# Performance work log

Hardware: AMD Instinct MI355X
Metric: run time of the kernel (lower is better)

## Reference

```python
import jax, jax.numpy as jnp
import numpy as np

K = 20      # kNN neighbors
H = 4       # attention heads
EPS = 1e-5  # BatchNorm eps
NEG = 0.2   # LeakyReLU negative slope


def lrelu(x):
    return jnp.where(x >= 0, x, NEG * x)


def bn(x, g, b):
    # eval-mode BatchNorm: running_mean=0, running_var=1
    return x * (g / jnp.sqrt(1.0 + EPS)) + b


def knn_idx(x):
    # x: (B, N, C) -> (B, N, K) indices of K nearest neighbors (incl. self)
    inner = -2.0 * jnp.einsum('bnc,bmc->bnm', x, x)
    xx = jnp.sum(x * x, axis=-1)
    pd = -xx[:, :, None] - inner - xx[:, None, :]  # negative squared distance
    return jax.lax.top_k(pd, K)[1]


def edge_conv(x, w, g, b):
    # EdgeConv: gather kNN features, cat(nbr-ctr, ctr), 1x1 conv, BN, LeakyReLU, max over K
    idx = knn_idx(x)                                   # (B,N,K)
    nbr = jax.vmap(lambda f, i: f[i])(x, idx)          # (B,N,K,C)
    ctr = jnp.broadcast_to(x[:, :, None, :], nbr.shape)
    e = jnp.concatenate([nbr - ctr, ctr], axis=-1)     # (B,N,K,2C)
    h = lrelu(bn(jnp.einsum('bnkc,oc->bnko', e, w), g, b))
    return jnp.max(h, axis=2)                          # (B,N,Cout)


def mha(x, w_in, b_in, w_out, b_out):
    # Faithful to source: (B,N,E) fed to nn.MultiheadAttention with batch_first=False,
    # so seq length L=B and batch=N (attention mixes across the batch axis).
    L, Nb, E = x.shape
    d = E // H
    qkv = x @ w_in.T + b_in
    q, k, v = jnp.split(qkv, 3, axis=-1)
    q = q.reshape(L, Nb, H, d) * (1.0 / np.sqrt(d))
    k = k.reshape(L, Nb, H, d)
    v = v.reshape(L, Nb, H, d)
    a = jax.nn.softmax(jnp.einsum('lnhd,mnhd->nhlm', q, k), axis=-1)
    o = jnp.einsum('nhlm,mnhd->lnhd', a, v).reshape(L, Nb, E)
    return o @ w_out.T + b_out


def setup_inputs():
    ks = iter(jax.random.split(jax.random.key(0), 64))
    def rn(shape, s=0.05):
        return jax.random.normal(next(ks), shape, jnp.float32) * s
    def gamma(c):
        return 1.0 + rn((c,), 0.1)
    B, N = 8, 1024
    inp = {'x': rn((B, N, 3), 1.0)}
    for i, (ci, co) in enumerate([(6, 64), (128, 64), (128, 128), (256, 256)], 1):
        inp[f'w{i}'] = rn((co, ci)); inp[f'g{i}'] = gamma(co); inp[f'b{i}'] = rn((co,))
    for i, e in enumerate([64, 64, 128, 256], 1):
        inp[f'a{i}_wi'] = rn((3 * e, e)); inp[f'a{i}_bi'] = rn((3 * e,))
        inp[f'a{i}_wo'] = rn((e, e));     inp[f'a{i}_bo'] = rn((e,))
    inp['w5'] = rn((1024, 512)); inp['g5'] = gamma(1024); inp['b5'] = rn((1024,))
    inp['l1w'] = rn((512, 2048)); inp['g6'] = gamma(512); inp['b6'] = rn((512,))
    inp['l2w'] = rn((256, 512)); inp['l2b'] = rn((256,))
    inp['g7'] = gamma(256); inp['b7'] = rn((256,))
    inp['l3w'] = rn((40, 256)); inp['l3b'] = rn((40,))
    return inp


def reference(x, w1, g1, b1, a1_wi, a1_bi, a1_wo, a1_bo,
              w2, g2, b2, a2_wi, a2_bi, a2_wo, a2_bo,
              w3, g3, b3, a3_wi, a3_bi, a3_wo, a3_bo,
              w4, g4, b4, a4_wi, a4_bi, a4_wo, a4_bo,
              w5, g5, b5, l1w, g6, b6, l2w, l2b, g7, b7, l3w, l3b):
    x1 = edge_conv(x, w1, g1, b1)
    x1 = mha(x1, a1_wi, a1_bi, a1_wo, a1_bo) + x1
    x2 = edge_conv(x1, w2, g2, b2)
    x2 = mha(x2, a2_wi, a2_bi, a2_wo, a2_bo) + x2
    x3 = edge_conv(x2, w3, g3, b3)
    x3 = mha(x3, a3_wi, a3_bi, a3_wo, a3_bo) + x3
    x4 = edge_conv(x3, w4, g4, b4)
    x4 = mha(x4, a4_wi, a4_bi, a4_wo, a4_bo) + x4
    h = lrelu(bn(jnp.concatenate([x1, x2, x3, x4], axis=-1) @ w5.T, g5, b5))  # (B,N,1024)
    feat = jnp.concatenate([jnp.max(h, axis=1), jnp.mean(h, axis=1)], axis=-1)  # (B,2048)
    h = lrelu(bn(feat @ l1w.T, g6, b6))
    h = lrelu(bn(h @ l2w.T + l2b, g7, b7))  # dropout is eval-mode identity
    return h @ l3w.T + l3b  # (B, 40)
```

## Files before the change

kernel.cpp:

```cpp
#include <hip/hip_runtime.h>
#include <hip/hip_bf16.h>

#define B_ 8
#define N_ 1024
#define K_ 20
#define BN_ (B_*N_)

#define BN_SCALE 0.9999950000374997f

typedef __attribute__((ext_vector_type(8))) short short8;
typedef __attribute__((ext_vector_type(4))) float f32x4;

__device__ __forceinline__ float US2F(unsigned short u) {
    union { unsigned u; float f; } c; c.u = ((unsigned)u) << 16; return c.f;
}
__device__ __forceinline__ unsigned short F2BF(float f) {
    union { float f; unsigned u; } c; c.f = f;
    unsigned r = c.u + 0x7FFF + ((c.u >> 16) & 1);
    return (unsigned short)(r >> 16);
}

__device__ __forceinline__ void ldsld16(const unsigned short* g, unsigned short* l) {
    __builtin_amdgcn_global_load_lds(
        (const __attribute__((address_space(1))) void*)g,
        (__attribute__((address_space(3))) void*)l, 16, 0, 0);
}

struct DetP { const unsigned short* g[7]; };
__device__ __forceinline__ int det_isbf(const DetP& dp) {
    int cnt = 0;
    #pragma unroll
    for (int i = 0; i < 7; i++) {
        float v = US2F(dp.g[i][0]);
        if (v > 0.5f && v < 1.5f) cnt++;
    }
    return cnt >= 4;
}

struct TPar { const void* src; void* dst; int O, I, blk0, mode; };
struct TList { TPar p[44]; };
struct TrP { const void* src; float* dst; int O, I, bx, blk0; };

__global__ __launch_bounds__(256) void k_prep(TList tl, int nent,
                                              TrP q0, TrP q1, TrP q2,
                                              int nbp, int nbtr,
                                              const void* x0, DetP dp,
                                              unsigned short* __restrict__ xa,
                                              unsigned short* __restrict__ xb,
                                              float* __restrict__ xx1) {
    __shared__ int sbf;
    if (threadIdx.x == 0) sbf = det_isbf(dp);
    __syncthreads();
    const int isbf = sbf;
    auto ld0 = [&](int idx) {
        return isbf ? US2F(((const unsigned short*)x0)[idx])
                    : ((const float*)x0)[idx];
    };
    const int bid = blockIdx.x;
    if (bid >= nbp + nbtr) {
        int blk = bid - nbp - nbtr;
        if (blk >= (BN_ * 32) / 256) {
            int i = (blk - (BN_ * 32) / 256) * 256 + threadIdx.x;
            if (i >= BN_) return;
            float s = 0.f;
            #pragma unroll
            for (int c = 0; c < 3; c++) { float v = ld0(i * 3 + c); s += v * v; }
            xx1[i] = s;
            return;
        }
        const int e = blk * 256 + threadIdx.x;
        const int i = e >> 5, p = e & 31;
        unsigned short va = 0, vb = 0;
        if (p < 9) {
            const int seg = p / 3, c = p - seg * 3;
            const float v = ld0(i * 3 + c);
            const unsigned short h = F2BF(v);
            const unsigned short l = F2BF(v - US2F(h));
            va = (seg == 1) ? l : h;
            vb = (seg < 2) ? h : l;
        }
        xa[e] = va; xb[e] = vb;
        return;
    }
    if (bid >= nbp) {
        int blk = bid - nbp;
        TrP p = q0;
        if (blk >= q2.blk0) p = q2; else if (blk >= q1.blk0) p = q1;
        blk -= p.blk0;
        const int tx = threadIdx.x & 31, ty = threadIdx.x >> 5;
        const int bi = blk % p.bx, bo = blk / p.bx;
        const int i0 = bi * 32, o0 = bo * 32;
        __shared__ float s[32][33];
        #pragma unroll
        for (int r = 0; r < 4; r++) {
            const int o = o0 + ty + r * 8, i = i0 + tx;
            if (o < p.O && i < p.I) {
                const size_t e = (size_t)o * p.I + i;
                s[ty + r * 8][tx] = isbf ? US2F(((const unsigned short*)p.src)[e])
                                         : ((const float*)p.src)[e];
            }
        }
        __syncthreads();
        #pragma unroll
        for (int r = 0; r < 4; r++) {
            const int i = i0 + ty + r * 8, o = o0 + tx;
            if (i < p.I && o < p.O) p.dst[(size_t)i * p.O + o] = s[tx][ty + r * 8];
        }
        return;
    }
    int blk = bid;
    int wi = 0;
    for (int j = nent - 1; j >= 0; j--) { if (blk >= tl.p[j].blk0) { wi = j; break; } }
    const TPar p = tl.p[wi];
    int e = (blk - p.blk0) * 256 + threadIdx.x;
    int n = p.O * p.I;
    if (e >= n) return;
    if (p.mode == 4) { ((float*)p.dst)[e] = 0.f; return; }
    int o = e / p.I, i = e - o * p.I;
    float v = isbf ? US2F(((const unsigned short*)p.src)[e])
                   : ((const float*)p.src)[e];
    if (p.mode == 0) {
        ((float*)p.dst)[(size_t)i * p.O + o] = v;
    } else if (p.mode == 2) {
        ((unsigned short*)p.dst)[e] = F2BF(v);
    } else {
        const int C = p.I >> 1;
        if (i < C) ((unsigned short*)p.dst)[(size_t)o * C + i] = F2BF(v);
        else       ((unsigned short*)p.dst)[(size_t)(p.O + o) * C + (i - C)] = F2BF(v);
    }
}

template<int KP, int TM, int TN>
__global__ __launch_bounds__(256) void k_pdm(const unsigned short* __restrict__ xa,
                                             const unsigned short* __restrict__ xb,
                                             const float* __restrict__ xx,
                                             float* __restrict__ pd) {
    const int b = blockIdx.z;
    const int rb = blockIdx.x * TM, cb = blockIdx.y * TN;
    const unsigned short* Ab = xa + (size_t)b * N_ * KP;
    const unsigned short* Bb = xb + (size_t)b * N_ * KP;
    const float* xxb = xx + (size_t)b * N_;
    const int t = threadIdx.x;
    __shared__ __align__(16) unsigned short As[2][TM * 32];
    __shared__ __align__(16) unsigned short Bs[2][TN * 32];
    const int w = t >> 6, lane = t & 63;
    constexpr int QR = TM / 2, QC = TN / 2;
    constexpr int MR = QR / 16, NR = QC / 16;
    const int wr = (w & 1) * QR, wc = (w >> 1) * QC;
    const int fr = lane & 15, q = lane >> 4;
    f32x4 acc[MR][NR] = {};

    auto STAGE = [&](int buf, int k0) {
        constexpr int AT = TM * 4;
        #pragma unroll
        for (int R = 0; R < (AT + 255) / 256; R++) {
            const int G = t + R * 256;
            if (AT >= (R + 1) * 256 || G < AT) {
                const int m = G >> 2, gs = (G & 3) ^ ((m >> 1) & 3);
                ldsld16(&Ab[(size_t)(rb + m) * KP + k0 + gs * 8], &As[buf][w * 512 + R * 2048]);
            }
        }
        constexpr int BT = TN * 4;
        #pragma unroll
        for (int R = 0; R < (BT + 255) / 256; R++) {
            const int G = t + R * 256;
            if (BT >= (R + 1) * 256 || G < BT) {
                const int n = G >> 2, gs = (G & 3) ^ ((n >> 1) & 3);
                ldsld16(&Bb[(size_t)(cb + n) * KP + k0 + gs * 8], &Bs[buf][w * 512 + R * 2048]);
            }
        }
    };

    constexpr int NT = KP / 32;
    STAGE(0, 0);
    asm volatile("s_waitcnt vmcnt(0)" ::: "memory");
    __builtin_amdgcn_s_barrier();
    int cur = 0;
    for (int ts = 0; ts < NT; ++ts) {
        if (ts + 1 < NT) STAGE(cur ^ 1, (ts + 1) * 32);
        short8 af[MR], bfr[NR];
        #pragma unroll
        for (int mi = 0; mi < MR; mi++) {
            const int r = wr + mi * 16 + fr;
            af[mi] = *reinterpret_cast<const short8*>(&As[cur][r * 32 + ((q ^ ((r >> 1) & 3)) << 3)]);
        }
        #pragma unroll
        for (int ni = 0; ni < NR; ni++) {
            const int r = wc + ni * 16 + fr;
            bfr[ni] = *reinterpret_cast<const short8*>(&Bs[cur][r * 32 + ((q ^ ((r >> 1) & 3)) << 3)]);
        }
        #pragma unroll
        for (int mi = 0; mi < MR; mi++) {
            #pragma unroll
            for (int ni = 0; ni < NR; ni++)
                acc[mi][ni] = __builtin_amdgcn_mfma_f32_16x16x32_bf16(af[mi], bfr[ni], acc[mi][ni], 0, 0, 0);
        }
        asm volatile("s_waitcnt vmcnt(0)" ::: "memory");
        __builtin_amdgcn_s_barrier();
        cur ^= 1;
    }
    float* pdb = pd + (size_t)b * N_ * N_;
    const int cr = (lane >> 4) * 4, cc = lane & 15;
    #pragma unroll
    for (int mi = 0; mi < MR; mi++) {
        #pragma unroll
        for (int ni = 0; ni < NR; ni++) {
            #pragma unroll
            for (int r = 0; r < 4; r++) {
                const int row = rb + wr + mi * 16 + cr + r;
                const int col = cb + wc + ni * 16 + cc;
                pdb[(size_t)row * N_ + col] = 2.f * acc[mi][ni][r] - xxb[col];
            }
        }
    }
}

__device__ __forceinline__ void sel_dev(const float* __restrict__ pd,
                                        int* __restrict__ idx, int blk) {
    const int w = threadIdx.x >> 6, lane = threadIdx.x & 63;
    const int i = blk * 4 + w;
    const int b = i >> 10;
    const float* row = pd + (size_t)b * N_ * N_ + (size_t)(i & 1023) * N_;
    unsigned key[16];
    #pragma unroll
    for (int q = 0; q < 16; q++) {
        const int j = q * 64 + lane;
        unsigned bits = __float_as_uint(row[j]);
        bits = (bits & 0x80000000u) ? ~bits : (bits | 0x80000000u);
        key[q] = (bits & 0xFFFFFC00u) | (unsigned)(N_ - 1 - j);
    }
    int myj = 0;
    for (int kk = 0; kk < K_; kk++) {
        unsigned m = key[0];
        #pragma unroll
        for (int u = 1; u < 16; u++) m = key[u] > m ? key[u] : m;
        #pragma unroll
        for (int s = 1; s < 64; s <<= 1) {
            unsigned o = (unsigned)__shfl_xor((int)m, s, 64);
            m = o > m ? o : m;
        }
        const int j = N_ - 1 - (int)(m & 1023u);
        if (lane == kk) myj = j;
        #pragma unroll
        for (int u = 0; u < 16; u++)
            if (key[u] == m) key[u] = 0u;
    }
    if (lane < K_) idx[(size_t)i * K_ + lane] = myj;
}

template<int KD, int NC, int TM, int TN, bool CATA, bool POOL, int SPLIT>
__device__ __forceinline__ void gemm_dev(int bx, int by,
                                         const unsigned short* __restrict__ A,
                                         const unsigned short* __restrict__ A2,
                                         const unsigned short* __restrict__ A3,
                                         const unsigned short* __restrict__ A4,
                                         const unsigned short* __restrict__ Bw,
                                         const float* __restrict__ bias,
                                         const float* __restrict__ resid,
                                         float* __restrict__ Cout,
                                         float* __restrict__ Cz, int yco,
                                         int scale_cols, float qs,
                                         const float* __restrict__ gamma,
                                         const float* __restrict__ beta,
                                         unsigned short* __restrict__ obf,
                                         unsigned* __restrict__ pmaxu,
                                         float* __restrict__ psum,
                                         unsigned short* __restrict__ sxa,
                                         unsigned short* __restrict__ sxb,
                                         float* __restrict__ xxo) {
    const int t = threadIdx.x;
    const int rb = bx * TM, cb = by * TN;
    const int w = t >> 6, lane = t & 63;
    constexpr int QR = TM / 2, QC = TN / 2;
    constexpr int MR = QR / 16, NR = QC / 16;
    const int wr = (w & 1) * QR, wc = (w >> 1) * QC;
    const int fr = lane & 15, q = lane >> 4, fq = q * 8;
    f32x4 acc[MR][NR] = {};
    if constexpr (KD % 32 == 0) {
        __shared__ __align__(16) unsigned short As[2][TM * 32];
        __shared__ __align__(16) unsigned short Bs[2][TN * 32];
        auto STAGE = [&](int buf, int k0) {
            const unsigned short* Asrc = A; int AC = KD, ac0 = k0;
            if constexpr (CATA) {
                if (k0 >= 256)      { Asrc = A4; AC = 256; ac0 = k0 - 256; }
                else if (k0 >= 128) { Asrc = A3; AC = 128; ac0 = k0 - 128; }
                else if (k0 >= 64)  { Asrc = A2; AC = 64;  ac0 = k0 - 64; }
                else                { Asrc = A;  AC = 64;  ac0 = k0; }
            }
            constexpr int AT = TM * 4;
            #pragma unroll
            for (int R = 0; R < (AT + 255) / 256; R++) {
                const int G = t + R * 256;
                if (AT >= (R + 1) * 256 || G < AT) {
                    const int m = G >> 2, gs = (G & 3) ^ ((m >> 1) & 3);
                    ldsld16(&Asrc[(size_t)(rb + m) * AC + ac0 + gs * 8], &As[buf][w * 512 + R * 2048]);
                }
            }
            constexpr int BT = TN * 4;
            #pragma unroll
            for (int R = 0; R < (BT + 255) / 256; R++) {
                const int G = t + R * 256;
                if (BT >= (R + 1) * 256 || G < BT) {
                    const int n = G >> 2, gs = (G & 3) ^ ((n >> 1) & 3);
                    ldsld16(&Bw[(size_t)(cb + n) * KD + k0 + gs * 8], &Bs[buf][w * 512 + R * 2048]);
                }
            }
        };
        constexpr int NT = KD / 32;
        STAGE(0, 0);
        asm volatile("s_waitcnt vmcnt(0)" ::: "memory");
        __builtin_amdgcn_s_barrier();
        int cur = 0;
        for (int ts = 0; ts < NT; ++ts) {
            if (ts + 1 < NT) STAGE(cur ^ 1, (ts + 1) * 32);
            short8 af[MR], bfr[NR];
            #pragma unroll
            for (int mi = 0; mi < MR; mi++) {
                const int r = wr + mi * 16 + fr;
                af[mi] = *reinterpret_cast<const short8*>(&As[cur][r * 32 + ((q ^ ((r >> 1) & 3)) << 3)]);
            }
            #pragma unroll
            for (int ni = 0; ni < NR; ni++) {
                const int r = wc + ni * 16 + fr;
                bfr[ni] = *reinterpret_cast<const short8*>(&Bs[cur][r * 32 + ((q ^ ((r >> 1) & 3)) << 3)]);
            }
            #pragma unroll
            for (int mi = 0; mi < MR; mi++) {
                #pragma unroll
                for (int ni = 0; ni < NR; ni++)
                    acc[mi][ni] = __builtin_amdgcn_mfma_f32_16x16x32_bf16(af[mi], bfr[ni], acc[mi][ni], 0, 0, 0);
            }
            asm volatile("s_waitcnt vmcnt(0)" ::: "memory");
            __builtin_amdgcn_s_barrier();
            cur ^= 1;
        }
    } else {
        __shared__ __align__(16) unsigned short As[TM * 40];
        __shared__ __align__(16) unsigned short Bs[TN * 40];
        for (int k0 = 0; k0 < KD; k0 += 32) {
            __syncthreads();
            #pragma unroll
            for (int u = t; u < TM * 4; u += 256) {
                const int m = u >> 2, c = (u & 3) * 8;
                #pragma unroll
                for (int j = 0; j < 8; j++) {
                    const int kk = k0 + c + j;
                    As[m * 40 + c + j] = (kk < KD) ? A[(size_t)(rb + m) * KD + kk] : (unsigned short)0;
                }
            }
            #pragma unroll
            for (int u = t; u < TN * 4; u += 256) {
                const int n = u >> 2, c = (u & 3) * 8;
                const int gn = cb + n;
                if (gn < NC) {
                    #pragma unroll
                    for (int j = 0; j < 8; j++) {
                        const int kk = k0 + c + j;
                        Bs[n * 40 + c + j] = (kk < KD) ? Bw[(size_t)gn * KD + kk] : (unsigned short)0;
                    }
                } else {
                    short8 z = {};
                    *reinterpret_cast<short8*>(&Bs[n * 40 + c]) = z;
                }
            }
            __syncthreads();
            short8 af[MR], bfr[NR];
            #pragma unroll
            for (int mi = 0; mi < MR; mi++)
                af[mi] = *reinterpret_cast<const short8*>(&As[(wr + mi * 16 + fr) * 40 + fq]);
            #pragma unroll
            for (int ni = 0; ni < NR; ni++)
                bfr[ni] = *reinterpret_cast<const short8*>(&Bs[(wc + ni * 16 + fr) * 40 + fq]);
            #pragma unroll
            for (int mi = 0; mi < MR; mi++) {
                #pragma unroll
                for (int ni = 0; ni < NR; ni++)
                    acc[mi][ni] = __builtin_amdgcn_mfma_f32_16x16x32_bf16(af[mi], bfr[ni], acc[mi][ni], 0, 0, 0);
            }
        }
    }
    const int cr = (lane >> 4) * 4, cc = lane & 15;
    if constexpr (POOL) {
        const int bidx = rb >> 10;
        #pragma unroll
        for (int ni = 0; ni < NR; ni++) {
            const int col = cb + wc + ni * 16 + cc;
            const float gm = gamma[col] * BN_SCALE, bt = beta[col];
            float sm = 0.f, mxv = -3e38f;
            #pragma unroll
            for (int mi = 0; mi < MR; mi++) {
                #pragma unroll
                for (int r = 0; r < 4; r++) {
                    float v = acc[mi][ni][r] * gm + bt;
                    v = v >= 0.f ? v : 0.2f * v;
                    sm += v; mxv = fmaxf(mxv, v);
                }
            }
            sm += __shfl_xor(sm, 16, 64);
            sm += __shfl_xor(sm, 32, 64);
            mxv = fmaxf(mxv, __shfl_xor(mxv, 16, 64));
            mxv = fmaxf(mxv, __shfl_xor(mxv, 32, 64));
            if (lane < 16) {
                atomicAdd(&psum[bidx * 1024 + col], sm);
                unsigned tb = __float_as_uint(mxv);
                tb = (tb & 0x80000000u) ? ~tb : (tb | 0x80000000u);
                atomicMax(&pmaxu[bidx * 1024 + col], tb);
            }
        }
    } else {
        float sx[MR][4] = {};
        #pragma unroll
        for (int mi = 0; mi < MR; mi++) {
            #pragma unroll
            for (int ni = 0; ni < NR; ni++) {
                #pragma unroll
                for (int r = 0; r < 4; r++) {
                    const int row = rb + wr + mi * 16 + cr + r;
                    const int col = cb + wc + ni * 16 + cc;
                    if (col < NC) {
                        float v = acc[mi][ni][r] + (bias ? bias[col] : 0.f);
                        if (col < scale_cols) v *= qs;
                        if (resid) v += resid[(size_t)row * NC + col];
                        if (gamma) {
                            v = v * (gamma[col] * BN_SCALE) + beta[col];
                            v = v >= 0.f ? v : 0.2f * v;
                        }
                        if (yco > 0) {
                            if (col < yco) Cout[(size_t)row * yco + col] = v;
                            else           Cz[(size_t)row * yco + (col - yco)] = v;
                        } else {
                            Cout[(size_t)row * NC + col] = v;
                        }
                        if (obf) obf[(size_t)row * NC + col] = F2BF(v);
                        if constexpr (SPLIT > 0) {
                            constexpr int KP2 = 3 * SPLIT;
                            const unsigned short h = F2BF(v);
                            const unsigned short l = F2BF(v - US2F(h));
                            sxa[(size_t)row * KP2 + 0 * SPLIT + col] = h;
                            sxa[(size_t)row * KP2 + 1 * SPLIT + col] = l;
                            sxa[(size_t)row * KP2 + 2 * SPLIT + col] = h;
                            sxb[(size_t)row * KP2 + 0 * SPLIT + col] = h;
                            sxb[(size_t)row * KP2 + 1 * SPLIT + col] = h;
                            sxb[(size_t)row * KP2 + 2 * SPLIT + col] = l;
                            sx[mi][r] += v * v;
                        }
                    }
                }
            }
        }
        if constexpr (SPLIT > 0) {
            #pragma unroll
            for (int mi = 0; mi < MR; mi++) {
                #pragma unroll
                for (int r = 0; r < 4; r++) {
                    float s = sx[mi][r];
                    s += __shfl_xor(s, 1, 64);
                    s += __shfl_xor(s, 2, 64);
                    s += __shfl_xor(s, 4, 64);
                    s += __shfl_xor(s, 8, 64);
                    if ((lane & 15) == 0)
                        atomicAdd(&xxo[rb + wr + mi * 16 + cr + r], s);
                }
            }
        }
    }
}

template<int KD, int NC, int TM, int TN, bool CATA = false, bool POOL = false, int SPLIT = 0>
__global__ __launch_bounds__(256) void k_gemmb(const unsigned short* __restrict__ A,
                                               const unsigned short* __restrict__ A2,
                                               const unsigned short* __restrict__ A3,
                                               const unsigned short* __restrict__ A4,
                                               const unsigned short* __restrict__ Bw,
                                               const float* __restrict__ bias,
                                               const float* __restrict__ resid,
                                               float* __restrict__ Cout,
                                               int scale_cols, float qs,
                                               const float* __restrict__ gamma,
                                               const float* __restrict__ beta,
                                               unsigned short* __restrict__ obf,
                                               unsigned* __restrict__ pmaxu,
                                               float* __restrict__ psum,
                                               unsigned short* __restrict__ sxa,
                                               unsigned short* __restrict__ sxb,
                                               float* __restrict__ xxo) {
    gemm_dev<KD, NC, TM, TN, CATA, POOL, SPLIT>(blockIdx.x, blockIdx.y,
        A, A2, A3, A4, Bw, bias, resid, Cout, nullptr, 0, scale_cols, qs, gamma, beta,
        obf, pmaxu, psum, sxa, sxb, xxo);
}

template<int KD, int NC, int TM, int TN>
__global__ __launch_bounds__(256) void k_selyz(const float* __restrict__ pd,
                                               int* __restrict__ idx, int selb, int gx,
                                               const unsigned short* __restrict__ A,
                                               const unsigned short* __restrict__ Bw,
                                               float* __restrict__ Cy,
                                               float* __restrict__ Cz, int yco) {
    if ((int)blockIdx.x < selb) { sel_dev(pd, idx, blockIdx.x); return; }
    const int g = blockIdx.x - selb;
    gemm_dev<KD, NC, TM, TN, false, false, 0>(g % gx, g / gx,
        A, nullptr, nullptr, nullptr, Bw, nullptr, nullptr, Cy, Cz, yco, 0, 1.f,
        nullptr, nullptr, nullptr, nullptr, nullptr, nullptr, nullptr, nullptr);
}

template<int CO>
__global__ __launch_bounds__(256) void k_edgemax(const float* __restrict__ y,
                                                 const float* __restrict__ z,
                                                 const int* __restrict__ idx,
                                                 const float* __restrict__ g,
                                                 const float* __restrict__ bb,
                                                 float* __restrict__ out,
                                                 unsigned short* __restrict__ outb) {
    constexpr int TPP = CO / 4;
    constexpr int PPB = 256 / TPP;
    const int t = threadIdx.x;
    const int p = t / TPP;
    const int cw = (t % TPP) * 4;
    const int batch = blockIdx.x & 7;
    const int within = blockIdx.x >> 3;
    const int i0 = batch * N_ + within * PPB;
    const int bbase = batch << 10;
    __shared__ int sidx[PPB][K_];
    for (int u = t; u < PPB * K_; u += 256) {
        int pp = u / K_, kk = u - pp * K_;
        sidx[pp][kk] = idx[(size_t)(i0 + pp) * K_ + kk];
    }
    __syncthreads();
    const int ig = i0 + p;
    float4 m = {-3e38f, -3e38f, -3e38f, -3e38f};
    #pragma unroll 4
    for (int k = 0; k < K_; k++) {
        const int jg = bbase + sidx[p][k];
        const float4 yv = *reinterpret_cast<const float4*>(&y[(size_t)jg * CO + cw]);
        m.x = fmaxf(m.x, yv.x); m.y = fmaxf(m.y, yv.y);
        m.z = fmaxf(m.z, yv.z); m.w = fmaxf(m.w, yv.w);
    }
    const float4 yi = *reinterpret_cast<const float4*>(&y[(size_t)ig * CO + cw]);
    const float4 zi = *reinterpret_cast<const float4*>(&z[(size_t)ig * CO + cw]);
    const float4 gv = *reinterpret_cast<const float4*>(&g[cw]);
    const float4 bv = *reinterpret_cast<const float4*>(&bb[cw]);
    float vals[4] = {m.x - yi.x + zi.x, m.y - yi.y + zi.y,
                     m.z - yi.z + zi.z, m.w - yi.w + zi.w};
    float gs[4] = {gv.x, gv.y, gv.z, gv.w};
    float bs[4] = {bv.x, bv.y, bv.z, bv.w};
    float4 o;
    float* op = &o.x;
    #pragma unroll
    for (int j = 0; j < 4; j++) {
        float h = vals[j] * (gs[j] * BN_SCALE) + bs[j];
        op[j] = h >= 0.f ? h : 0.2f * h;
    }
    *reinterpret_cast<float4*>(&out[(size_t)ig * CO + cw]) = o;
    #pragma unroll
    for (int j = 0; j < 4; j++) outb[(size_t)ig * CO + cw + j] = F2BF(op[j]);
}

template<int E>
__global__ __launch_bounds__(256) void k_attn(const float* __restrict__ qkv,
                                              unsigned short* __restrict__ o) {
    constexpr int H = 4, D = E / H, L = 8;
    const int n = blockIdx.x;
    const int t = threadIdx.x;
    const int h = t >> 6, lane = t & 63;
    __shared__ float sq[L][3 * E];
    __shared__ float so[L][E];
    for (int u = t; u < L * 3 * E; u += 256) {
        int l = u / (3 * E), r = u - l * (3 * E);
        sq[l][r] = qkv[(size_t)(l * N_ + n) * (3 * E) + r];
    }
    __syncthreads();
    const int l = lane >> 3, m = lane & 7;
    float s = 0.f;
    #pragma unroll 8
    for (int dd = 0; dd < D; dd++)
        s += sq[l][h * D + dd] * sq[m][E + h * D + dd];
    float mx = s;
    #pragma unroll
    for (int st = 1; st < 8; st <<= 1) mx = fmaxf(mx, __shfl_xor(mx, st, 64));
    float e = expf(s - mx);
    float sum = e;
    #pragma unroll
    for (int st = 1; st < 8; st <<= 1) sum += __shfl_xor(sum, st, 64);
    const float p = e / sum;
    float pm[8];
    #pragma unroll
    for (int mm = 0; mm < 8; mm++) pm[mm] = __shfl(p, (lane & 56) | mm, 64);
    #pragma unroll
    for (int j = 0; j < D / 8; j++) {
        const int dd = m + 8 * j;
        float a = 0.f;
        #pragma unroll
        for (int mm = 0; mm < 8; mm++) a += pm[mm] * sq[mm][2 * E + h * D + dd];
        so[l][h * D + dd] = a;
    }
    __syncthreads();
    for (int u = t; u < L * E; u += 256) {
        int l2 = u / E, e2 = u - l2 * E;
        o[(size_t)(l2 * N_ + n) * E + e2] = F2BF(so[l2][e2]);
    }
}

__global__ __launch_bounds__(256) void k_fc1(const unsigned* __restrict__ pmaxu,
                                             const float* __restrict__ psum,
                                             const float* __restrict__ l1wT,
                                             const float* __restrict__ g6, const float* __restrict__ b6,
                                             float* __restrict__ f1) {
    int oc = blockIdx.x, b = blockIdx.y, t = threadIdx.x;
    __shared__ float fin[2048];
    __shared__ float ps[4][64];
    for (int u = t; u < 2048; u += 256) {
        float v;
        if (u < 1024) {
            unsigned tb = pmaxu[b * 1024 + u];
            unsigned bits = (tb & 0x80000000u) ? (tb & 0x7FFFFFFFu) : ~tb;
            v = __uint_as_float(bits);
        } else {
            v = psum[b * 1024 + (u - 1024)] * (1.f / 1024.f);
        }
        fin[u] = v;
    }
    __syncthreads();
    int ol = t & 63, kc = t >> 6;
    int o = oc * 64 + ol;
    float acc = 0.f;
    for (int c = kc * 512; c < kc * 512 + 512; c++) acc += fin[c] * l1wT[(size_t)c * 512 + o];
    ps[kc][ol] = acc;
    __syncthreads();
    if (t < 64) {
        int oo = oc * 64 + t;
        float a = ps[0][t] + ps[1][t] + ps[2][t] + ps[3][t];
        float h = a * (g6[oo] * BN_SCALE) + b6[oo];
        f1[b * 512 + oo] = h >= 0.f ? h : 0.2f * h;
    }
}

__global__ __launch_bounds__(256) void k_fc23(const float* __restrict__ f1, const float* __restrict__ l2wT,
                                              const float* __restrict__ l2b,
                                              const float* __restrict__ g7, const float* __restrict__ b7,
                                              const float* __restrict__ l3wT, const float* __restrict__ l3b,
                                              void* __restrict__ out, DetP dp) {
    int b = blockIdx.x, t = threadIdx.x;
    __shared__ float fin[512];
    __shared__ float f2s[256];
    __shared__ int sbf;
    if (t == 0) sbf = det_isbf(dp);
    for (int u = t; u < 512; u += 256) fin[u] = f1[b * 512 + u];
    __syncthreads();
    {
        float acc = 0.f;
        for (int c = 0; c < 512; c++) acc += fin[c] * l2wT[(size_t)c * 256 + t];
        acc += l2b[t];
        float h = acc * (g7[t] * BN_SCALE) + b7[t];
        f2s[t] = h >= 0.f ? h : 0.2f * h;
    }
    __syncthreads();
    if (t < 40) {
        float acc = 0.f;
        for (int c = 0; c < 256; c++) acc += f2s[c] * l3wT[(size_t)c * 40 + t];
        acc += l3b[t];
        if (sbf) ((__hip_bfloat16*)out)[b * 40 + t] = __float2bfloat16(acc);
        else     ((float*)out)[b * 40 + t] = acc;
    }
}

extern "C" void kernel_launch(void* const* d_in, const int* in_sizes, int n_in,
                              void* d_out, int out_size, void* d_ws, size_t ws_size,
                              hipStream_t stream) {
    auto us = [&](int i) { return (const unsigned short*)d_in[i]; };

    float* ws = (float*)d_ws;
    size_t off = 0;
    auto A = [&](size_t n) { float* p = ws + off; off += (n + 3) & ~(size_t)3; return p; };
    auto AU = [&](size_t n) { return (unsigned short*)A((n + 1) / 2); };
    float* x1   = A((size_t)BN_ * 64);
    float* x2   = A((size_t)BN_ * 64);
    float* x3   = A((size_t)BN_ * 128);
    float* x4   = A((size_t)BN_ * 256);
    float* pd   = A((size_t)BN_ * 1024);
    float* f1   = A(8 * 512);
    float* xx   = A(4 * BN_);
    int*   idx  = (int*)A((size_t)BN_ * K_);
    float* qkvw = A((size_t)BN_ * 768);
    unsigned short* xf0b = AU((size_t)BN_ * 3);
    unsigned short* x1b  = AU((size_t)BN_ * 64);
    unsigned short* x2b  = AU((size_t)BN_ * 64);
    unsigned short* x3b  = AU((size_t)BN_ * 128);
    unsigned short* x4b  = AU((size_t)BN_ * 256);
    unsigned short* owb  = AU((size_t)BN_ * 256);
    unsigned* pmaxu = (unsigned*)A(8 * 1024);
    float*    psum  = A(8 * 1024);
    unsigned short* w1yzb = AU(128 * 3);
    unsigned short* w2yzb = AU(128 * 64);
    unsigned short* w3yzb = AU(256 * 64);
    unsigned short* w4yzb = AU(512 * 128);
    unsigned short* a1wib = AU(192 * 64);  unsigned short* a1wob = AU(64 * 64);
    unsigned short* a2wib = AU(192 * 64);  unsigned short* a2wob = AU(64 * 64);
    unsigned short* a3wib = AU(384 * 128); unsigned short* a3wob = AU(128 * 128);
    unsigned short* a4wib = AU(768 * 256); unsigned short* a4wob = AU(256 * 256);
    unsigned short* w5b   = AU(1024 * 512);
    float* l1wT  = A(2048 * 512);
    float* l2wT  = A(512 * 256);
    float* l3wT  = A(256 * 40);
    float* g1f = A(64);   float* b1f = A(64);
    float* g2f = A(64);   float* b2f = A(64);
    float* g3f = A(128);  float* b3f = A(128);
    float* g4f = A(256);  float* b4f = A(256);
    float* bi1 = A(192);  float* bo1 = A(64);
    float* bi2 = A(192);  float* bo2 = A(64);
    float* bi3 = A(384);  float* bo3 = A(128);
    float* bi4 = A(768);  float* bo4 = A(256);
    float* g5f = A(1024); float* b5f = A(1024);
    float* g6f = A(512);  float* b6f = A(512);
    float* l2bf = A(256);
    float* g7f = A(256);  float* b7f = A(256);
    float* l3bf = A(40);

    float* xx1 = xx;              float* xx2 = xx + BN_;
    float* xx3 = xx + 2 * BN_;    float* xx4 = xx + 3 * BN_;

    unsigned short* xa = (unsigned short*)qkvw;
    unsigned short* xb = (unsigned short*)qkvw + (size_t)BN_ * 384;
    float* yy = qkvw;
    float* zz = qkvw + (size_t)BN_ * 256;

    DetP dp{{us(2), us(5), us(8), us(11), us(30), us(33), us(37)}};

    TList tl; int nb = 0; int k = 0;
    auto add = [&](int i, void* dst, int O, int I, int mode) {
        tl.p[k].src = d_in[i]; tl.p[k].dst = dst; tl.p[k].O = O; tl.p[k].I = I;
        tl.p[k].blk0 = nb; tl.p[k].mode = mode;
        nb += (O * I + 255) / 256; k++;
    };
    add(0,  xf0b,  BN_ * 3, 1, 2);
    add(0,  pmaxu, 16384, 1, 4);
    add(0,  xx2,   3 * BN_, 1, 4);
    add(1,  w1yzb, 64, 6, 3);
    add(4,  w2yzb, 64, 128, 3);
    add(7,  w3yzb, 128, 128, 3);
    add(10, w4yzb, 256, 256, 3);
    add(13, a1wib, 192, 64, 2);
    add(15, a1wob, 64, 64, 2);
    add(17, a2wib, 192, 64, 2);
    add(19, a2wob, 64, 64, 2);
    add(21, a3wib, 384, 128, 2);
    add(23, a3wob, 128, 128, 2);
    add(25, a4wib, 768, 256, 2);
    add(27, a4wob, 256, 256, 2);
    add(29, w5b,   1024, 512, 2);
    add(2,  g1f, 64, 1, 0);   add(3,  b1f, 64, 1, 0);
    add(5,  g2f, 64, 1, 0);   add(6,  b2f, 64, 1, 0);
    add(8,  g3f, 128, 1, 0);  add(9,  b3f, 128, 1, 0);
    add(11, g4f, 256, 1, 0);  add(12, b4f, 256, 1, 0);
    add(14, bi1, 192, 1, 0);  add(16, bo1, 64, 1, 0);
    add(18, bi2, 192, 1, 0);  add(20, bo2, 64, 1, 0);
    add(22, bi3, 384, 1, 0);  add(24, bo3, 128, 1, 0);
    add(26, bi4, 768, 1, 0);  add(28, bo4, 256, 1, 0);
    add(30, g5f, 1024, 1, 0); add(31, b5f, 1024, 1, 0);
    add(33, g6f, 512, 1, 0);  add(34, b6f, 512, 1, 0);
    add(36, l2bf, 256, 1, 0);
    add(37, g7f, 256, 1, 0);  add(38, b7f, 256, 1, 0);
    add(40, l3bf, 40, 1, 0);

    TrP tp1{d_in[32], l1wT, 512, 2048, 2048 / 32, 0};
    TrP tp2{d_in[35], l2wT, 256, 512,  512 / 32,  (2048 / 32) * (512 / 32)};
    TrP tp3{d_in[39], l3wT, 40,  256,  256 / 32,  tp2.blk0 + (512 / 32) * (256 / 32)};
    const int trblocks = tp3.blk0 + (256 / 32) * ((40 + 31) / 32);
    const int splblocks = (BN_ * 32) / 256 + 32;
    k_prep<<<nb + trblocks + splblocks, 256, 0, stream>>>(
        tl, k, tp1, tp2, tp3, nb, trblocks, d_in[0], dp, xa, xb, xx1);

    const dim3 pdmg(8, 8, 8);
    const unsigned short* N0 = nullptr;
    unsigned short* U0 = nullptr;
    unsigned* NU = nullptr; float* NF = nullptr;

    k_pdm<32, 128, 128><<<pdmg, 256, 0, stream>>>(xa, xb, xx1, pd);
    k_selyz<3, 128, 64, 64><<<2048 + 256, 256, 0, stream>>>(pd, idx, 2048, 128, xf0b, w1yzb, yy, zz, 64);
    k_edgemax<64><<<BN_ / 16, 256, 0, stream>>>(yy, zz, idx, g1f, b1f, x1, x1b);
    k_gemmb<64, 192, 64, 64><<<dim3(128, 3), 256, 0, stream>>>(x1b, N0, N0, N0, a1wib, bi1, nullptr, qkvw, 64, 0.25f, nullptr, nullptr, nullptr, NU, NF, U0, U0, NF);
    k_attn<64><<<N_, 256, 0, stream>>>(qkvw, owb);
    k_gemmb<64, 64, 64, 64, false, false, 64><<<dim3(128, 1), 256, 0, stream>>>(owb, N0, N0, N0, a1wob, bo1, x1, x1, 0, 1.f, nullptr, nullptr, x1b, NU, NF, xa, xb, xx2);

    k_pdm<192, 128, 128><<<pdmg, 256, 0, stream>>>(xa, xb, xx2, pd);
    k_selyz<64, 128, 64, 64><<<2048 + 256, 256, 0, stream>>>(pd, idx, 2048, 128, x1b, w2yzb, yy, zz, 64);
    k_edgemax<64><<<BN_ / 16, 256, 0, stream>>>(yy, zz, idx, g2f, b2f, x2, x2b);
    k_gemmb<64, 192, 64, 64><<<dim3(128, 3), 256, 0, stream>>>(x2b, N0, N0, N0, a2wib, bi2, nullptr, qkvw, 64, 0.25f, nullptr, nullptr, nullptr, NU, NF, U0, U0, NF);
    k_attn<64><<<N_, 256, 0, stream>>>(qkvw, owb);
    k_gemmb<64, 64, 64, 64, false, false, 64><<<dim3(128, 1), 256, 0, stream>>>(owb, N0, N0, N0, a2wob, bo2, x2, x2, 0, 1.f, nullptr, nullptr, x2b, NU, NF, xa, xb, xx3);

    k_pdm<192, 128, 128><<<pdmg, 256, 0, stream>>>(xa, xb, xx3, pd);
    k_selyz<64, 256, 64, 64><<<2048 + 512, 256, 0, stream>>>(pd, idx, 2048, 128, x2b, w3yzb, yy, zz, 128);
    k_edgemax<128><<<BN_ / 8, 256, 0, stream>>>(yy, zz, idx, g3f, b3f, x3, x3b);
    k_gemmb<128, 384, 64, 128><<<dim3(128, 3), 256, 0, stream>>>(x3b, N0, N0, N0, a3wib, bi3, nullptr, qkvw, 128, 0.17677669529663687f, nullptr, nullptr, nullptr, NU, NF, U0, U0, NF);
    k_attn<128><<<N_, 256, 0, stream>>>(qkvw, owb);
    k_gemmb<128, 128, 64, 64, false, false, 128><<<dim3(128, 2), 256, 0, stream>>>(owb, N0, N0, N0, a3wob, bo3, x3, x3, 0, 1.f, nullptr, nullptr, x3b, NU, NF, xa, xb, xx4);

    k_pdm<384, 128, 128><<<pdmg, 256, 0, stream>>>(xa, xb, xx4, pd);
    k_selyz<128, 512, 128, 128><<<2048 + 256, 256, 0, stream>>>(pd, idx, 2048, 64, x3b, w4yzb, yy, zz, 256);
    k_edgemax<256><<<BN_ / 4, 256, 0, stream>>>(yy, zz, idx, g4f, b4f, x4, x4b);
    k_gemmb<256, 768, 128, 128><<<dim3(64, 6), 256, 0, stream>>>(x4b, N0, N0, N0, a4wib, bi4, nullptr, qkvw, 256, 0.125f, nullptr, nullptr, nullptr, NU, NF, U0, U0, NF);
    k_attn<256><<<N_, 256, 0, stream>>>(qkvw, owb);
    k_gemmb<256, 256, 64, 128><<<dim3(128, 2), 256, 0, stream>>>(owb, N0, N0, N0, a4wob, bo4, x4, x4, 0, 1.f, nullptr, nullptr, x4b, NU, NF, U0, U0, NF);

    k_gemmb<512, 1024, 128, 128, true, true><<<dim3(64, 8), 256, 0, stream>>>(
        x1b, x2b, x3b, x4b, w5b, nullptr, nullptr, nullptr, 0, 1.f, g5f, b5f, nullptr, pmaxu, psum, U0, U0, NF);
    k_fc1<<<dim3(8, 8), 256, 0, stream>>>(pmaxu, psum, l1wT, g6f, b6f, f1);
    k_fc23<<<8, 256, 0, stream>>>(f1, l2wT, l2bf, g7f, b7f, l3wT, l3bf, d_out, dp);
}
```

Before: 510.8 us.

## Remap block indices so consecutive blocks land on XCDs by batch for L2 locality

Block IDs in the distance-matrix, selection, projection and attention GEMM kernels are remapped so the low 3 bits select the batch (or an eighth of the row range). Blocks dispatched round-robin across the 8 XCDs then keep each batch's data within one XCD's L2, aiming to cut cross-XCD cache misses. The batch-4 QKV GEMM tile also changes from 128x128 to 64x128 with twice the blocks. The remapping adds a little index arithmetic and relies on the dispatch order to XCDs.

```diff
diff --git a/kernel.cpp b/kernel.cpp
--- a/kernel.cpp
+++ b/kernel.cpp
@@ -135,8 +135,10 @@
                                              const unsigned short* __restrict__ xb,
                                              const float* __restrict__ xx,
                                              float* __restrict__ pd) {
-    const int b = blockIdx.z;
-    const int rb = blockIdx.x * TM, cb = blockIdx.y * TN;
+    const int bid = blockIdx.x;
+    const int b = bid & 7;
+    const int tt = bid >> 3;
+    const int rb = (tt >> 3) * TM, cb = (tt & 7) * TN;
     const unsigned short* Ab = xa + (size_t)b * N_ * KP;
     const unsigned short* Bb = xb + (size_t)b * N_ * KP;
     const float* xxb = xx + (size_t)b * N_;
@@ -218,8 +220,8 @@
 __device__ __forceinline__ void sel_dev(const float* __restrict__ pd,
                                         int* __restrict__ idx, int blk) {
     const int w = threadIdx.x >> 6, lane = threadIdx.x & 63;
-    const int i = blk * 4 + w;
-    const int b = i >> 10;
+    const int b = blk & 7;
+    const int i = (b << 10) + ((blk >> 3) << 2) + w;
     const float* row = pd + (size_t)b * N_ * N_ + (size_t)(i & 1023) * N_;
     unsigned key[16];
     #pragma unroll
@@ -466,7 +468,7 @@
     }
 }
 
-template<int KD, int NC, int TM, int TN, bool CATA = false, bool POOL = false, int SPLIT = 0>
+template<int KD, int NC, int TM, int TN, bool CATA = false, bool POOL = false, int SPLIT = 0, bool AFF = false>
 __global__ __launch_bounds__(256) void k_gemmb(const unsigned short* __restrict__ A,
                                                const unsigned short* __restrict__ A2,
                                                const unsigned short* __restrict__ A3,
@@ -484,7 +486,9 @@
                                                unsigned short* __restrict__ sxa,
                                                unsigned short* __restrict__ sxb,
                                                float* __restrict__ xxo) {
-    gemm_dev<KD, NC, TM, TN, CATA, POOL, SPLIT>(blockIdx.x, blockIdx.y,
+    int bx = blockIdx.x;
+    if constexpr (AFF) bx = (bx & 7) * (gridDim.x >> 3) + (bx >> 3);
+    gemm_dev<KD, NC, TM, TN, CATA, POOL, SPLIT>(bx, blockIdx.y,
         A, A2, A3, A4, Bw, bias, resid, Cout, nullptr, 0, scale_cols, qs, gamma, beta,
         obf, pmaxu, psum, sxa, sxb, xxo);
 }
@@ -498,7 +502,11 @@
                                                float* __restrict__ Cz, int yco) {
     if ((int)blockIdx.x < selb) { sel_dev(pd, idx, blockIdx.x); return; }
     const int g = blockIdx.x - selb;
-    gemm_dev<KD, NC, TM, TN, false, false, 0>(g % gx, g / gx,
+    const int batch = g & 7, rem = g >> 3;
+    const int rpb = gx >> 3;
+    const int bx = batch * rpb + rem % rpb;
+    const int by = rem / rpb;
+    gemm_dev<KD, NC, TM, TN, false, false, 0>(bx, by,
         A, nullptr, nullptr, nullptr, Bw, nullptr, nullptr, Cy, Cz, yco, 0, 1.f,
         nullptr, nullptr, nullptr, nullptr, nullptr, nullptr, nullptr, nullptr);
 }
@@ -769,40 +777,39 @@
     k_prep<<<nb + trblocks + splblocks, 256, 0, stream>>>(
         tl, k, tp1, tp2, tp3, nb, trblocks, d_in[0], dp, xa, xb, xx1);
 
-    const dim3 pdmg(8, 8, 8);
     const unsigned short* N0 = nullptr;
     unsigned short* U0 = nullptr;
     unsigned* NU = nullptr; float* NF = nullptr;
 
-    k_pdm<32, 128, 128><<<pdmg, 256, 0, stream>>>(xa, xb, xx1, pd);
+    k_pdm<32, 128, 128><<<512, 256, 0, stream>>>(xa, xb, xx1, pd);
     k_selyz<3, 128, 64, 64><<<2048 + 256, 256, 0, stream>>>(pd, idx, 2048, 128, xf0b, w1yzb, yy, zz, 64);
     k_edgemax<64><<<BN_ / 16, 256, 0, stream>>>(yy, zz, idx, g1f, b1f, x1, x1b);
-    k_gemmb<64, 192, 64, 64><<<dim3(128, 3), 256, 0, stream>>>(x1b, N0, N0, N0, a1wib, bi1, nullptr, qkvw, 64, 0.25f, nullptr, nullptr, nullptr, NU, NF, U0, U0, NF);
+    k_gemmb<64, 192, 64, 64, false, false, 0, true><<<dim3(128, 3), 256, 0, stream>>>(x1b, N0, N0, N0, a1wib, bi1, nullptr, qkvw, 64, 0.25f, nullptr, nullptr, nullptr, NU, NF, U0, U0, NF);
     k_attn<64><<<N_, 256, 0, stream>>>(qkvw, owb);
-    k_gemmb<64, 64, 64, 64, false, false, 64><<<dim3(128, 1), 256, 0, stream>>>(owb, N0, N0, N0, a1wob, bo1, x1, x1, 0, 1.f, nullptr, nullptr, x1b, NU, NF, xa, xb, xx2);
-
-    k_pdm<192, 128, 128><<<pdmg, 256, 0, stream>>>(xa, xb, xx2, pd);
+    k_gemmb<64, 64, 64, 64, false, false, 64, true><<<dim3(128, 1), 256, 0, stream>>>(owb, N0, N0, N0, a1wob, bo1, x1, x1, 0, 1.f, nullptr, nullptr, x1b, NU, NF, xa, xb, xx2);
+
+    k_pdm<192, 128, 128><<<512, 256, 0, stream>>>(xa, xb, xx2, pd);
     k_selyz<64, 128, 64, 64><<<2048 + 256, 256, 0, stream>>>(pd, idx, 2048, 128, x1b, w2yzb, yy, zz, 64);
     k_edgemax<64><<<BN_ / 16, 256, 0, stream>>>(yy, zz, idx, g2f, b2f, x2, x2b);
-    k_gemmb<64, 192, 64, 64><<<dim3(128, 3), 256, 0, stream>>>(x2b, N0, N0, N0, a2wib, bi2, nullptr, qkvw, 64, 0.25f, nullptr, nullptr, nullptr, NU, NF, U0, U0, NF);
+    k_gemmb<64, 192, 64, 64, false, false, 0, true><<<dim3(128, 3), 256, 0, stream>>>(x2b, N0, N0, N0, a2wib, bi2, nullptr, qkvw, 64, 0.25f, nullptr, nullptr, nullptr, NU, NF, U0, U0, NF);
     k_attn<64><<<N_, 256, 0, stream>>>(qkvw, owb);
-    k_gemmb<64, 64, 64, 64, false, false, 64><<<dim3(128, 1), 256, 0, stream>>>(owb, N0, N0, N0, a2wob, bo2, x2, x2, 0, 1.f, nullptr, nullptr, x2b, NU, NF, xa, xb, xx3);
-
-    k_pdm<192, 128, 128><<<pdmg, 256, 0, stream>>>(xa, xb, xx3, pd);
+    k_gemmb<64, 64, 64, 64, false, false, 64, true><<<dim3(128, 1), 256, 0, stream>>>(owb, N0, N0, N0, a2wob, bo2, x2, x2, 0, 1.f, nullptr, nullptr, x2b, NU, NF, xa, xb, xx3);
+
+    k_pdm<192, 128, 128><<<512, 256, 0, stream>>>(xa, xb, xx3, pd);
     k_selyz<64, 256, 64, 64><<<2048 + 512, 256, 0, stream>>>(pd, idx, 2048, 128, x2b, w3yzb, yy, zz, 128);
     k_edgemax<128><<<BN_ / 8, 256, 0, stream>>>(yy, zz, idx, g3f, b3f, x3, x3b);
-    k_gemmb<128, 384, 64, 128><<<dim3(128, 3), 256, 0, stream>>>(x3b, N0, N0, N0, a3wib, bi3, nullptr, qkvw, 128, 0.17677669529663687f, nullptr, nullptr, nullptr, NU, NF, U0, U0, NF);
+    k_gemmb<128, 384, 64, 128, false, false, 0, true><<<dim3(128, 3), 256, 0, stream>>>(x3b, N0, N0, N0, a3wib, bi3, nullptr, qkvw, 128, 0.17677669529663687f, nullptr, nullptr, nullptr, NU, NF, U0, U0, NF);
     k_attn<128><<<N_, 256, 0, stream>>>(qkvw, owb);
-    k_gemmb<128, 128, 64, 64, false, false, 128><<<dim3(128, 2), 256, 0, stream>>>(owb, N0, N0, N0, a3wob, bo3, x3, x3, 0, 1.f, nullptr, nullptr, x3b, NU, NF, xa, xb, xx4);
-
-    k_pdm<384, 128, 128><<<pdmg, 256, 0, stream>>>(xa, xb, xx4, pd);
+    k_gemmb<128, 128, 64, 64, false, false, 128, true><<<dim3(128, 2), 256, 0, stream>>>(owb, N0, N0, N0, a3wob, bo3, x3, x3, 0, 1.f, nullptr, nullptr, x3b, NU, NF, xa, xb, xx4);
+
+    k_pdm<384, 128, 128><<<512, 256, 0, stream>>>(xa, xb, xx4, pd);
     k_selyz<128, 512, 128, 128><<<2048 + 256, 256, 0, stream>>>(pd, idx, 2048, 64, x3b, w4yzb, yy, zz, 256);
     k_edgemax<256><<<BN_ / 4, 256, 0, stream>>>(yy, zz, idx, g4f, b4f, x4, x4b);
-    k_gemmb<256, 768, 128, 128><<<dim3(64, 6), 256, 0, stream>>>(x4b, N0, N0, N0, a4wib, bi4, nullptr, qkvw, 256, 0.125f, nullptr, nullptr, nullptr, NU, NF, U0, U0, NF);
+    k_gemmb<256, 768, 64, 128, false, false, 0, true><<<dim3(128, 6), 256, 0, stream>>>(x4b, N0, N0, N0, a4wib, bi4, nullptr, qkvw, 256, 0.125f, nullptr, nullptr, nullptr, NU, NF, U0, U0, NF);
     k_attn<256><<<N_, 256, 0, stream>>>(qkvw, owb);
-    k_gemmb<256, 256, 64, 128><<<dim3(128, 2), 256, 0, stream>>>(owb, N0, N0, N0, a4wob, bo4, x4, x4, 0, 1.f, nullptr, nullptr, x4b, NU, NF, U0, U0, NF);
-
-    k_gemmb<512, 1024, 128, 128, true, true><<<dim3(64, 8), 256, 0, stream>>>(
+    k_gemmb<256, 256, 64, 128, false, false, 0, true><<<dim3(128, 2), 256, 0, stream>>>(owb, N0, N0, N0, a4wob, bo4, x4, x4, 0, 1.f, nullptr, nullptr, x4b, NU, NF, U0, U0, NF);
+
+    k_gemmb<512, 1024, 128, 128, true, true, 0, true><<<dim3(64, 8), 256, 0, stream>>>(
         x1b, x2b, x3b, x4b, w5b, nullptr, nullptr, nullptr, 0, 1.f, g5f, b5f, nullptr, pmaxu, psum, U0, U0, NF);
     k_fc1<<<dim3(8, 8), 256, 0, stream>>>(pmaxu, psum, l1wT, g6f, b6f, f1);
     k_fc23<<<8, 256, 0, stream>>>(f1, l2wT, l2bf, g7f, b7f, l3wT, l3bf, d_out, dp);
```

After: 501.7 us. About the same (-1.8%).
